# Optimization experiments

Hardware: AMD Instinct MI355X
Metric: run time of the kernel (lower is better)

## Reference

```python
import jax, jax.numpy as jnp
import numpy as np

B, T, D = 16, 1024, 768
H = 12
HD = D // H
MLP = 3072


def _layernorm(x, g, b, eps=1e-5):
    mu = jnp.mean(x, axis=-1, keepdims=True)
    var = jnp.var(x, axis=-1, keepdims=True)
    return (x - mu) * jax.lax.rsqrt(var + eps) * g + b


def setup_inputs() -> dict:
    key = jax.random.key(0)
    ks = jax.random.split(key, 12)
    s_d = 1.0 / np.sqrt(D)
    s_m = 1.0 / np.sqrt(MLP)
    return {
        "x": jax.random.normal(ks[0], (B, T, D), dtype=jnp.float32),
        "Wq": jax.random.uniform(ks[1], (D, D), jnp.float32, -s_d, s_d),
        "bq": jnp.zeros((D,), jnp.float32),
        "Wk": jax.random.uniform(ks[2], (D, D), jnp.float32, -s_d, s_d),
        "bk": jnp.zeros((D,), jnp.float32),
        "Wv": jax.random.uniform(ks[3], (D, D), jnp.float32, -s_d, s_d),
        "bv": jnp.zeros((D,), jnp.float32),
        "Wo": jax.random.uniform(ks[4], (D, D), jnp.float32, -s_d, s_d),
        "bo": jnp.zeros((D,), jnp.float32),
        "ln1_g": jnp.ones((D,), jnp.float32),
        "ln1_b": jnp.zeros((D,), jnp.float32),
        "ln2_g": jnp.ones((D,), jnp.float32),
        "ln2_b": jnp.zeros((D,), jnp.float32),
        "W1": jax.random.uniform(ks[5], (D, MLP), jnp.float32, -s_d, s_d),
        "b1": jnp.zeros((MLP,), jnp.float32),
        "W2": jax.random.uniform(ks[6], (MLP, D), jnp.float32, -s_m, s_m),
        "b2": jnp.zeros((D,), jnp.float32),
    }


def reference(x, Wq, bq, Wk, bk, Wv, bv, Wo, bo, ln1_g, ln1_b, ln2_g, ln2_b, W1, b1, W2, b2):
    h = _layernorm(x, ln1_g, ln1_b)
    # QKV projections -> [B, H, T, HD]
    q = (h @ Wq + bq).reshape(B, T, H, HD).transpose(0, 2, 1, 3)
    k = (h @ Wk + bk).reshape(B, T, H, HD).transpose(0, 2, 1, 3)
    v = (h @ Wv + bv).reshape(B, T, H, HD).transpose(0, 2, 1, 3)
    # NOTE: original divides by sqrt(input_dim), not sqrt(head_dim)
    scores = jnp.einsum('bhtf,bhjf->bhtj', q, k) / jnp.sqrt(jnp.float32(D))
    score = jax.nn.softmax(scores, axis=-1)
    attn = jnp.einsum('bhij,bhjf->bihf', score, v)  # [B, T, H, HD]
    attn_out = attn.reshape(B, T, D) @ Wo + bo
    out = attn_out + x
    h2 = _layernorm(out, ln2_g, ln2_b)
    # MLP: Linear -> GELU -> Linear -> GELU (GELU after 2nd linear is in the source)
    m = jax.nn.gelu(h2 @ W1 + b1, approximate=False)
    m = jax.nn.gelu(m @ W2 + b2, approximate=False)
    return m + out
```

## Files before the change

kernel.cpp:

```cpp
#include <hip/hip_runtime.h>
#include <hip/hip_bf16.h>
#include <math.h>

#define D_MODEL 768
#define T_SEQ   1024
#define B_BATCH 16
#define MLP_DIM 3072
#define M_ROWS  (B_BATCH * T_SEQ)

typedef __attribute__((ext_vector_type(8))) __bf16          bf16x8;
typedef __attribute__((ext_vector_type(4))) __bf16          bf16x4;
typedef __attribute__((ext_vector_type(4))) float           f32x4;

__device__ __forceinline__ float bf2f(unsigned short u) {
  union { unsigned int u; float f; } w; w.u = ((unsigned int)u) << 16; return w.f;
}
__device__ __forceinline__ unsigned short f2bf(float f) {
  union { float f; unsigned int u; } w; w.f = f;
  unsigned int r = (w.u + 0x7fffu + ((w.u >> 16) & 1u)) >> 16;
  return (unsigned short)r;
}
__device__ __forceinline__ float gelu_f(float x) {
  return 0.5f * x * (1.0f + erff(x * 0.70710678118654752f));
}
__device__ __forceinline__ void gload16(const void* g, void* l) {
  __builtin_amdgcn_global_load_lds(
      (const __attribute__((address_space(1))) unsigned int*)g,
      (__attribute__((address_space(3))) unsigned int*)l, 16, 0, 0);
}

__global__ void wtr_k(const float* __restrict__ src,
                      unsigned short* __restrict__ dst, int R, int C) {
  __shared__ float t[32][33];
  const int c0 = blockIdx.x * 32, r0 = blockIdx.y * 32;
  const int tx = threadIdx.x, ty = threadIdx.y;
  #pragma unroll
  for (int j = 0; j < 32; j += 8)
    t[ty + j][tx] = src[(size_t)(r0 + ty + j) * C + (c0 + tx)];
  __syncthreads();
  #pragma unroll
  for (int j = 0; j < 32; j += 8)
    dst[(size_t)(c0 + ty + j) * R + (r0 + tx)] = f2bf(t[tx][ty + j]);
}

__global__ void bcat_k(const float* __restrict__ a, const float* __restrict__ b,
                       const float* __restrict__ c, float* __restrict__ o) {
  const int i = blockIdx.x * 256 + threadIdx.x;
  if (i < 768) { o[i] = a[i]; o[i + 768] = b[i]; o[i + 1536] = c[i]; }
}

template<int SRC_F32>
__global__ __launch_bounds__(256) void ln_k(const void* __restrict__ src,
    const float* __restrict__ g, const float* __restrict__ b,
    unsigned short* __restrict__ out) {
  const int row = blockIdx.x, tid = threadIdx.x;
  const size_t base = (size_t)row * D_MODEL;
  float v[3];
  #pragma unroll
  for (int i = 0; i < 3; ++i) {
    const int c = tid + (i << 8);
    v[i] = SRC_F32 ? ((const float*)src)[base + c]
                   : bf2f(((const unsigned short*)src)[base + c]);
  }
  float s  = v[0] + v[1] + v[2];
  float sq = v[0]*v[0] + v[1]*v[1] + v[2]*v[2];
  #pragma unroll
  for (int m = 32; m; m >>= 1) { s += __shfl_xor(s, m); sq += __shfl_xor(sq, m); }
  __shared__ float ps[4], pq[4];
  if ((tid & 63) == 0) { ps[tid >> 6] = s; pq[tid >> 6] = sq; }
  __syncthreads();
  s  = ps[0] + ps[1] + ps[2] + ps[3];
  sq = pq[0] + pq[1] + pq[2] + pq[3];
  const float mu  = s * (1.0f / 768.0f);
  const float var = sq * (1.0f / 768.0f) - mu * mu;
  const float inv = rsqrtf(var + 1e-5f);
  #pragma unroll
  for (int i = 0; i < 3; ++i) {
    const int c = tid + (i << 8);
    out[base + c] = f2bf((v[i] - mu) * inv * g[c] + b[c]);
  }
}

template<int EP>
__global__ __launch_bounds__(256) void gemm_k(
    const unsigned short* __restrict__ Au, const unsigned short* __restrict__ Btu,
    const float* __restrict__ bias, void* __restrict__ outv,
    const void* __restrict__ residv, void* __restrict__ aux,
    int M, int N, int K, int cb, int cgrp) {
  __shared__ __align__(16) __bf16 SMEM[2 * 2 * 128 * 32];
  auto As = (__bf16 (*)[128][32])(SMEM);
  auto Bs = (__bf16 (*)[128][32])(SMEM + 2 * 128 * 32);
  const __bf16* A  = (const __bf16*)Au;
  const __bf16* Bt = (const __bf16*)Btu;
  const int tid = threadIdx.x;
  const int lane = tid & 63, wid = tid >> 6;
  const int wr = wid >> 1, wc = wid & 1;
  const int gx = gridDim.x, gy = gridDim.y;
  const int bid = blockIdx.y * gx + blockIdx.x;
  const int xcd = bid & 7, idx = bid >> 3;
  const int rpx = gx >> 3;
  const int gsz = rpx * cgrp;
  const int grp = idx / gsz, rem = idx - grp * gsz;
  const int r = rem / cgrp, c = rem - r * cgrp + grp * cgrp;
  const int brow  = (xcd * rpx + r) * 128;
  const int bcolL = c * 128;
  const int bcol  = cb + bcolL;
  const int lr = lane & 15, lg = lane >> 4;
  f32x4 acc[4][4];
  #pragma unroll
  for (int m = 0; m < 4; ++m)
    #pragma unroll
    for (int n = 0; n < 4; ++n) acc[m][n] = (f32x4){0.f, 0.f, 0.f, 0.f};

  const int srow = (wid << 5) + (lane >> 2);
  const int scol = (lane & 3) << 3;
  const __bf16* gA = A  + (size_t)(brow  + srow) * K + scol;
  const __bf16* gB = Bt + (size_t)(bcolL + srow) * K + scol;

#define STAGE_(buf_, k0_) do {                                        \
    gload16(gA + (k0_),                   &As[buf_][(wid << 5)][0]);  \
    gload16(gA + (k0_) + 16 * (size_t)K,  &As[buf_][(wid << 5) + 16][0]); \
    gload16(gB + (k0_),                   &Bs[buf_][(wid << 5)][0]);  \
    gload16(gB + (k0_) + 16 * (size_t)K,  &Bs[buf_][(wid << 5) + 16][0]); \
  } while (0)

  STAGE_(0, 0);
  int cur = 0;
  for (int k0 = 0; k0 < K; k0 += 32, cur ^= 1) {
    if (k0 + 32 < K) {
      STAGE_(cur ^ 1, k0 + 32);
      asm volatile("s_waitcnt vmcnt(4)" ::: "memory");
    } else {
      asm volatile("s_waitcnt vmcnt(0)" ::: "memory");
    }
    __builtin_amdgcn_s_barrier();
    __builtin_amdgcn_sched_barrier(0);
    bf16x8 af[4], bfr[4];
    #pragma unroll
    for (int m = 0; m < 4; ++m) af[m]  = *(const bf16x8*)(&As[cur][wr*64 + m*16 + lr][lg*8]);
    #pragma unroll
    for (int n = 0; n < 4; ++n) bfr[n] = *(const bf16x8*)(&Bs[cur][wc*64 + n*16 + lr][lg*8]);
    #pragma unroll
    for (int m = 0; m < 4; ++m)
      #pragma unroll
      for (int n = 0; n < 4; ++n)
        acc[m][n] = __builtin_amdgcn_mfma_f32_16x16x32_bf16(af[m], bfr[n], acc[m][n], 0, 0, 0);
    asm volatile("s_waitcnt lgkmcnt(0)" ::: "memory");
    __builtin_amdgcn_sched_barrier(0);
    __builtin_amdgcn_s_barrier();
    __builtin_amdgcn_sched_barrier(0);
  }
#undef STAGE_

  const int seg = (EP == 5) ? (bcol / 768) : 0;
  unsigned short* qkvp = nullptr;
  if (EP == 5)
    qkvp = (seg == 0) ? (unsigned short*)outv
         : (seg == 1) ? (unsigned short*)residv : (unsigned short*)aux;

  if (EP == 5 && seg == 2) {
    #pragma unroll
    for (int n = 0; n < 4; ++n) {
      const int col = bcol + wc*64 + n*16 + lr;
      const float bv = bias[col];
      const int colLv = col - 1536;
      #pragma unroll
      for (int m = 0; m < 4; ++m) {
        const int row0 = brow + wr*64 + m*16 + lg*4;
        #pragma unroll
        for (int r2 = 0; r2 < 4; ++r2) {
          const int gr = row0 + r2;
          qkvp[(((size_t)(gr >> 10) * D_MODEL + colLv) << 10) + (gr & 1023)] =
              f2bf(acc[m][n][r2] + bv);
        }
      }
    }
  } else {
    float* Ep = (float*)SMEM + wid * 1280;
    #pragma unroll
    for (int p = 0; p < 4; ++p) {
      #pragma unroll
      for (int n = 0; n < 4; ++n) {
        const int col = bcol + wc*64 + n*16 + lr;
        const float bv = bias[col];
        f32x4 st;
        #pragma unroll
        for (int r2 = 0; r2 < 4; ++r2) {
          float v = acc[p][n][r2] + bv;
          if (EP == 1 || EP == 3) v = gelu_f(v);
          st[r2] = v;
        }
        *(f32x4*)(Ep + (n*16 + lr) * 20 + lg*4) = st;
      }
      #pragma unroll
      for (int i2 = 0; i2 < 2; ++i2) {
        const int rowL = i2*8 + (lane >> 3);
        const int colL = (lane & 7) * 8;
        const int grow = brow + wr*64 + p*16 + rowL;
        const int gcol = bcol + wc*64 + colL;
        float v[8];
        #pragma unroll
        for (int j = 0; j < 8; ++j) v[j] = Ep[(colL + j) * 20 + rowL];
        const size_t o = (size_t)grow * N + gcol;
        if (EP == 3) {
          const bf16x8 rv = *(const bf16x8*)((const __bf16*)residv + o);
          float* op = (float*)outv + o;
          float4 o0, o1;
          o0.x = v[0] + (float)rv[0]; o0.y = v[1] + (float)rv[1];
          o0.z = v[2] + (float)rv[2]; o0.w = v[3] + (float)rv[3];
          o1.x = v[4] + (float)rv[4]; o1.y = v[5] + (float)rv[5];
          o1.z = v[6] + (float)rv[6]; o1.w = v[7] + (float)rv[7];
          *(float4*)op = o0; *(float4*)(op + 4) = o1;
        } else if (EP == 2) {
          const float* rp = (const float*)residv + o;
          const float4 r0 = *(const float4*)rp, r1 = *(const float4*)(rp + 4);
          bf16x8 ov;
          ov[0] = (__bf16)(v[0] + r0.x); ov[1] = (__bf16)(v[1] + r0.y);
          ov[2] = (__bf16)(v[2] + r0.z); ov[3] = (__bf16)(v[3] + r0.w);
          ov[4] = (__bf16)(v[4] + r1.x); ov[5] = (__bf16)(v[5] + r1.y);
          ov[6] = (__bf16)(v[6] + r1.z); ov[7] = (__bf16)(v[7] + r1.w);
          *(bf16x8*)((__bf16*)outv + o) = ov;
        } else if (EP == 5) {
          bf16x8 ov;
          #pragma unroll
          for (int j = 0; j < 8; ++j) ov[j] = (__bf16)v[j];
          *(bf16x8*)((__bf16*)qkvp + (size_t)grow * 768 + (gcol - seg * 768)) = ov;
        } else {
          bf16x8 ov;
          #pragma unroll
          for (int j = 0; j < 8; ++j) ov[j] = (__bf16)v[j];
          *(bf16x8*)((__bf16*)outv + o) = ov;
        }
      }
    }
  }
}

__global__ __launch_bounds__(512) void attn_k(
    const unsigned short* qu, const unsigned short* __restrict__ ku,
    const unsigned short* __restrict__ vtu, unsigned short* attn) {
  __shared__ __align__(16) __bf16 Kl[64][72];
  __shared__ __align__(16) __bf16 Vl[64][72];
  __shared__ __align__(16) __bf16 Pl[8][16][72];
  const __bf16* qg  = (const __bf16*)qu;
  const __bf16* kg  = (const __bf16*)ku;
  const __bf16* vtg = (const __bf16*)vtu;
  const int bid = blockIdx.x;
  const int xcd = bid & 7, idx = bid >> 3;
  const int bh = xcd * 24 + (idx >> 2);
  const int b = bh / 12, h = bh % 12;
  const int q0 = (idx & 3) * 256;
  const int tid = threadIdx.x, lane = tid & 63, w = tid >> 6;
  const int lr = lane & 15, lg = lane >> 4;
  const float scale = 0.03608439182435161f;

  bf16x8 qa[2][2];
  #pragma unroll
  for (int g = 0; g < 2; ++g) {
    const int qrow = b * T_SEQ + q0 + w * 32 + g * 16 + lr;
    const __bf16* qp = qg + (size_t)qrow * D_MODEL + h * 64 + lg * 8;
    qa[g][0] = *(const bf16x8*)(qp);
    qa[g][1] = *(const bf16x8*)(qp + 32);
  }

  const __bf16* kb = kg  + (size_t)b * T_SEQ * D_MODEL + h * 64;
  const __bf16* vb = vtg + ((size_t)b * D_MODEL + h * 64) * T_SEQ;

  f32x4 o[2][4];
  float m_run[2] = {-1e30f, -1e30f}, l_run[2] = {0.f, 0.f};
  #pragma unroll
  for (int g = 0; g < 2; ++g)
    #pragma unroll
    for (int m = 0; m < 4; ++m) o[g][m] = (f32x4){0.f, 0.f, 0.f, 0.f};

  for (int kv0 = 0; kv0 < T_SEQ; kv0 += 64) {
    __syncthreads();
    {
      const int r = tid >> 3, c = (tid & 7) << 3;
      *(bf16x8*)(&Kl[r][c]) = *(const bf16x8*)(kb + (size_t)(kv0 + r) * D_MODEL + c);
      *(bf16x8*)(&Vl[r][c]) = *(const bf16x8*)(vb + (size_t)r * T_SEQ + kv0 + c);
    }
    __syncthreads();

    #pragma unroll
    for (int g = 0; g < 2; ++g) {
      f32x4 s[4];
      __builtin_amdgcn_s_setprio(1);
      #pragma unroll
      for (int m = 0; m < 4; ++m) {
        s[m] = (f32x4){0.f, 0.f, 0.f, 0.f};
        const bf16x8 kf0 = *(const bf16x8*)(&Kl[m*16 + lr][lg*8]);
        const bf16x8 kf1 = *(const bf16x8*)(&Kl[m*16 + lr][32 + lg*8]);
        s[m] = __builtin_amdgcn_mfma_f32_16x16x32_bf16(kf0, qa[g][0], s[m], 0, 0, 0);
        s[m] = __builtin_amdgcn_mfma_f32_16x16x32_bf16(kf1, qa[g][1], s[m], 0, 0, 0);
      }
      __builtin_amdgcn_s_setprio(0);
      float sv[4][4], tm = -1e30f;
      #pragma unroll
      for (int m = 0; m < 4; ++m)
        #pragma unroll
        for (int r = 0; r < 4; ++r) {
          sv[m][r] = s[m][r] * scale;
          tm = fmaxf(tm, sv[m][r]);
        }
      tm = fmaxf(tm, __shfl_xor(tm, 16));
      tm = fmaxf(tm, __shfl_xor(tm, 32));
      const float mn = fmaxf(m_run[g], tm);
      const float sc = __expf(m_run[g] - mn);
      float ts = 0.f;
      bf16x4 pk[4];
      #pragma unroll
      for (int m = 0; m < 4; ++m)
        #pragma unroll
        for (int r = 0; r < 4; ++r) {
          const float pp = __expf(sv[m][r] - mn);
          ts += pp;
          pk[m][r] = (__bf16)pp;
        }
      ts += __shfl_xor(ts, 16);
      ts += __shfl_xor(ts, 32);
      l_run[g] = l_run[g] * sc + ts;
      m_run[g] = mn;
      #pragma unroll
      for (int m = 0; m < 4; ++m)
        #pragma unroll
        for (int r = 0; r < 4; ++r) o[g][m][r] *= sc;
      #pragma unroll
      for (int m = 0; m < 4; ++m)
        *(bf16x4*)(&Pl[w][lr][16*m + 4*lg]) = pk[m];
      const bf16x8 pf0 = *(const bf16x8*)(&Pl[w][lr][lg*8]);
      const bf16x8 pf1 = *(const bf16x8*)(&Pl[w][lr][32 + lg*8]);
      __builtin_amdgcn_s_setprio(1);
      #pragma unroll
      for (int m = 0; m < 4; ++m) {
        const bf16x8 vf0 = *(const bf16x8*)(&Vl[m*16 + lr][lg*8]);
        const bf16x8 vf1 = *(const bf16x8*)(&Vl[m*16 + lr][32 + lg*8]);
        o[g][m] = __builtin_amdgcn_mfma_f32_16x16x32_bf16(vf0, pf0, o[g][m], 0, 0, 0);
        o[g][m] = __builtin_amdgcn_mfma_f32_16x16x32_bf16(vf1, pf1, o[g][m], 0, 0, 0);
      }
      __builtin_amdgcn_s_setprio(0);
    }
  }

  #pragma unroll
  for (int g = 0; g < 2; ++g) {
    const float inv = 1.0f / l_run[g];
    const int qrow = b * T_SEQ + q0 + w * 32 + g * 16 + lr;
    unsigned short* op = attn + (size_t)qrow * D_MODEL + h * 64;
    #pragma unroll
    for (int m = 0; m < 4; ++m) {
      bf16x4 ov;
      #pragma unroll
      for (int r = 0; r < 4; ++r) ov[r] = (__bf16)(o[g][m][r] * inv);
      *(bf16x4*)(op + 16*m + 4*lg) = ov;
    }
  }
}

extern "C" void kernel_launch(void* const* d_in, const int* in_sizes, int n_in,
                              void* d_out, int out_size, void* d_ws, size_t ws_size,
                              hipStream_t stream) {
  const float* x   = (const float*)d_in[0];
  const float* Wq  = (const float*)d_in[1];
  const float* bq  = (const float*)d_in[2];
  const float* Wk  = (const float*)d_in[3];
  const float* bk  = (const float*)d_in[4];
  const float* Wv  = (const float*)d_in[5];
  const float* bv  = (const float*)d_in[6];
  const float* Wo  = (const float*)d_in[7];
  const float* bo  = (const float*)d_in[8];
  const float* g1  = (const float*)d_in[9];
  const float* bt1 = (const float*)d_in[10];
  const float* g2  = (const float*)d_in[11];
  const float* bt2 = (const float*)d_in[12];
  const float* W1  = (const float*)d_in[13];
  const float* bb1 = (const float*)d_in[14];
  const float* W2  = (const float*)d_in[15];
  const float* bb2 = (const float*)d_in[16];

  const size_t SZ = (size_t)M_ROWS * D_MODEL * 2;
  char* wp = (char*)d_ws;
  unsigned short* wqkvT = (unsigned short*)wp; wp += (size_t)2304 * 768 * 2;
  unsigned short* woT   = (unsigned short*)wp; wp += (size_t)768 * 768 * 2;
  unsigned short* w1T   = (unsigned short*)wp; wp += (size_t)768 * 3072 * 2;
  unsigned short* w2T   = (unsigned short*)wp; wp += (size_t)768 * 3072 * 2;
  float*          bqkv  = (float*)wp;          wp += ((size_t)2304 * 4 + 255) & ~(size_t)255;
  unsigned short* kbuf  = (unsigned short*)wp; wp += SZ;
  unsigned short* vtb   = (unsigned short*)wp;
  unsigned short* res2  = kbuf;
  unsigned short* hid   = vtb;
  const size_t avail = ws_size - (size_t)(wp - (char*)d_ws);
  const int nch = (avail >= (size_t)M_ROWS * MLP_DIM * 2) ? 1
                : (avail >= (size_t)(M_ROWS / 2) * MLP_DIM * 2) ? 2 : 4;

  unsigned short* qd = (unsigned short*)d_out;
  unsigned short* h1 = qd + (size_t)M_ROWS * D_MODEL;
  unsigned short* h2 = h1;

  const dim3 tb(32, 8, 1);
  wtr_k<<<dim3(24, 24), tb, 0, stream>>>(Wq, wqkvT, 768, 768);
  wtr_k<<<dim3(24, 24), tb, 0, stream>>>(Wk, wqkvT + (size_t)768 * 768, 768, 768);
  wtr_k<<<dim3(24, 24), tb, 0, stream>>>(Wv, wqkvT + (size_t)1536 * 768, 768, 768);
  wtr_k<<<dim3(24, 24), tb, 0, stream>>>(Wo, woT, 768, 768);
  wtr_k<<<dim3(96, 24), tb, 0, stream>>>(W1, w1T, 768, 3072);
  wtr_k<<<dim3(24, 96), tb, 0, stream>>>(W2, w2T, 3072, 768);
  bcat_k<<<3, 256, 0, stream>>>(bq, bk, bv, bqkv);

  ln_k<1><<<M_ROWS, 256, 0, stream>>>(x, g1, bt1, h1);

  gemm_k<5><<<dim3(128, 18), 256, 0, stream>>>(h1, wqkvT, bqkv, qd, kbuf, vtb,
                                               M_ROWS, 2304, 768, 0, 9);

  attn_k<<<dim3(768), 512, 0, stream>>>(qd, kbuf, vtb, qd);

  gemm_k<2><<<dim3(128, 6), 256, 0, stream>>>(qd, woT, bo, res2, x, nullptr,
                                              M_ROWS, 768, 768, 0, 6);

  ln_k<0><<<M_ROWS, 256, 0, stream>>>(res2, g2, bt2, h2);

  const int CH = M_ROWS / nch;
  for (int c = 0; c < nch; ++c) {
    const size_t ro = (size_t)c * CH;
    gemm_k<1><<<dim3(CH / 128, 24), 256, 0, stream>>>(h2 + ro * 768, w1T, bb1,
        hid, nullptr, nullptr, CH, 3072, 768, 0, 12);
    gemm_k<3><<<dim3(CH / 128, 6), 256, 0, stream>>>(hid, w2T, bb2,
        (float*)d_out + ro * 768, res2 + ro * 768, nullptr, CH, 768, 3072, 0, 6);
  }
}
```

Baseline: 522.7 us.

## Enlarge GEMM tiles to 256x256 with 8 waves, K-step 64, swizzled LDS

The GEMM kernel now uses 256x256 output tiles computed by 512 threads (2x4 waves, each 128x64), a K-step of 64 per stage, and an XOR-swizzled LDS layout to avoid bank conflicts. It also raises wave priority around the MFMA block. All four GEMM launches are resized to match. The goal is more data reuse per byte loaded and fewer loop iterations. The cost is much higher register pressure (128 accumulator floats per lane), larger LDS use per block, and fewer blocks, which risks poor wave balance on the smaller GEMMs.

Result: faster. 508.3 us (-2.8%).

```diff
diff --git a/kernel.cpp b/kernel.cpp
--- a/kernel.cpp
+++ b/kernel.cpp
@@ -82,69 +82,95 @@
 }
 
 template<int EP>
-__global__ __launch_bounds__(256) void gemm_k(
+__global__ __launch_bounds__(512) void gemm_k(
     const unsigned short* __restrict__ Au, const unsigned short* __restrict__ Btu,
     const float* __restrict__ bias, void* __restrict__ outv,
     const void* __restrict__ residv, void* __restrict__ aux,
-    int M, int N, int K, int cb, int cgrp) {
-  __shared__ __align__(16) __bf16 SMEM[2 * 2 * 128 * 32];
-  auto As = (__bf16 (*)[128][32])(SMEM);
-  auto Bs = (__bf16 (*)[128][32])(SMEM + 2 * 128 * 32);
+    int M, int N, int K, int cgrp) {
+  __shared__ __align__(16) __bf16 SMEM[2 * 32768];
   const __bf16* A  = (const __bf16*)Au;
   const __bf16* Bt = (const __bf16*)Btu;
   const int tid = threadIdx.x;
-  const int lane = tid & 63, wid = tid >> 6;
-  const int wr = wid >> 1, wc = wid & 1;
+  const int lane = tid & 63, w = tid >> 6;
+  const int wr = w >> 2, wc = w & 3;
+  const int lr = lane & 15, lg = lane >> 4;
   const int gx = gridDim.x, gy = gridDim.y;
   const int bid = blockIdx.y * gx + blockIdx.x;
   const int xcd = bid & 7, idx = bid >> 3;
   const int rpx = gx >> 3;
   const int gsz = rpx * cgrp;
   const int grp = idx / gsz, rem = idx - grp * gsz;
-  const int r = rem / cgrp, c = rem - r * cgrp + grp * cgrp;
-  const int brow  = (xcd * rpx + r) * 128;
-  const int bcolL = c * 128;
-  const int bcol  = cb + bcolL;
-  const int lr = lane & 15, lg = lane >> 4;
-  f32x4 acc[4][4];
-  #pragma unroll
-  for (int m = 0; m < 4; ++m)
+  const int rb = rem / cgrp, cc2 = rem - rb * cgrp + grp * cgrp;
+  const int brow = (xcd * rpx + rb) * 256;
+  const int bcol = cc2 * 256;
+
+  f32x4 acc[8][4];
+  #pragma unroll
+  for (int m = 0; m < 8; ++m)
     #pragma unroll
     for (int n = 0; n < 4; ++n) acc[m][n] = (f32x4){0.f, 0.f, 0.f, 0.f};
 
-  const int srow = (wid << 5) + (lane >> 2);
-  const int scol = (lane & 3) << 3;
-  const __bf16* gA = A  + (size_t)(brow  + srow) * K + scol;
-  const __bf16* gB = Bt + (size_t)(bcolL + srow) * K + scol;
-
-#define STAGE_(buf_, k0_) do {                                        \
-    gload16(gA + (k0_),                   &As[buf_][(wid << 5)][0]);  \
-    gload16(gA + (k0_) + 16 * (size_t)K,  &As[buf_][(wid << 5) + 16][0]); \
-    gload16(gB + (k0_),                   &Bs[buf_][(wid << 5)][0]);  \
-    gload16(gB + (k0_) + 16 * (size_t)K,  &Bs[buf_][(wid << 5) + 16][0]); \
+  const int rrs = lane >> 2;
+  const int ccs = (lane & 3) << 3;
+  const int csw = ccs ^ ((rrs >> 3) << 4);
+  const __bf16* sA[4]; const __bf16* sB[4]; int dA[4], dB[4];
+  #pragma unroll
+  for (int g = 0; g < 4; ++g) {
+    const int s = g * 8 + w;
+    const int rsrc = (s >> 1) * 16 + rrs;
+    const int csrc = (s & 1) * 32 + csw;
+    sA[g] = A  + (size_t)(brow + rsrc) * K + csrc;
+    sB[g] = Bt + (size_t)(bcol + rsrc) * K + csrc;
+    dA[g] = s * 512;
+    dB[g] = 16384 + s * 512;
+  }
+
+#define STAGE_(buf_, k0_) do {                                     \
+    _Pragma("unroll")                                              \
+    for (int g = 0; g < 4; ++g) {                                  \
+      gload16(sA[g] + (k0_), &SMEM[(buf_) * 32768 + dA[g]]);       \
+      gload16(sB[g] + (k0_), &SMEM[(buf_) * 32768 + dB[g]]);       \
+    }                                                              \
   } while (0)
+
+  const int rbase = lr * 32 + ((lg << 3) ^ (((lr >> 3) & 1) << 4));
 
   STAGE_(0, 0);
   int cur = 0;
-  for (int k0 = 0; k0 < K; k0 += 32, cur ^= 1) {
-    if (k0 + 32 < K) {
-      STAGE_(cur ^ 1, k0 + 32);
-      asm volatile("s_waitcnt vmcnt(4)" ::: "memory");
+  for (int k0 = 0; k0 < K; k0 += 64, cur ^= 1) {
+    if (k0 + 64 < K) {
+      STAGE_(cur ^ 1, k0 + 64);
+      asm volatile("s_waitcnt vmcnt(8)" ::: "memory");
     } else {
       asm volatile("s_waitcnt vmcnt(0)" ::: "memory");
     }
     __builtin_amdgcn_s_barrier();
     __builtin_amdgcn_sched_barrier(0);
-    bf16x8 af[4], bfr[4];
-    #pragma unroll
-    for (int m = 0; m < 4; ++m) af[m]  = *(const bf16x8*)(&As[cur][wr*64 + m*16 + lr][lg*8]);
-    #pragma unroll
-    for (int n = 0; n < 4; ++n) bfr[n] = *(const bf16x8*)(&Bs[cur][wc*64 + n*16 + lr][lg*8]);
-    #pragma unroll
-    for (int m = 0; m < 4; ++m)
-      #pragma unroll
-      for (int n = 0; n < 4; ++n)
-        acc[m][n] = __builtin_amdgcn_mfma_f32_16x16x32_bf16(af[m], bfr[n], acc[m][n], 0, 0, 0);
+    const int bb = cur * 32768;
+    bf16x8 bfr[4][2];
+    #pragma unroll
+    for (int n = 0; n < 4; ++n)
+      #pragma unroll
+      for (int kk = 0; kk < 2; ++kk)
+        bfr[n][kk] = *(const bf16x8*)(&SMEM[bb + 16384 + ((wc*4 + n)*2 + kk)*512 + rbase]);
+    __builtin_amdgcn_s_setprio(1);
+    #pragma unroll
+    for (int mq = 0; mq < 2; ++mq) {
+      bf16x8 af[4][2];
+      #pragma unroll
+      for (int ml = 0; ml < 4; ++ml)
+        #pragma unroll
+        for (int kk = 0; kk < 2; ++kk)
+          af[ml][kk] = *(const bf16x8*)(&SMEM[bb + ((wr*8 + mq*4 + ml)*2 + kk)*512 + rbase]);
+      #pragma unroll
+      for (int ml = 0; ml < 4; ++ml)
+        #pragma unroll
+        for (int n = 0; n < 4; ++n) {
+          acc[mq*4+ml][n] = __builtin_amdgcn_mfma_f32_16x16x32_bf16(af[ml][0], bfr[n][0], acc[mq*4+ml][n], 0, 0, 0);
+          acc[mq*4+ml][n] = __builtin_amdgcn_mfma_f32_16x16x32_bf16(af[ml][1], bfr[n][1], acc[mq*4+ml][n], 0, 0, 0);
+        }
+    }
+    __builtin_amdgcn_s_setprio(0);
     asm volatile("s_waitcnt lgkmcnt(0)" ::: "memory");
     __builtin_amdgcn_sched_barrier(0);
     __builtin_amdgcn_s_barrier();
@@ -165,8 +191,8 @@
       const float bv = bias[col];
       const int colLv = col - 1536;
       #pragma unroll
-      for (int m = 0; m < 4; ++m) {
-        const int row0 = brow + wr*64 + m*16 + lg*4;
+      for (int m = 0; m < 8; ++m) {
+        const int row0 = brow + wr*128 + m*16 + lg*4;
         #pragma unroll
         for (int r2 = 0; r2 < 4; ++r2) {
           const int gr = row0 + r2;
@@ -176,9 +202,9 @@
       }
     }
   } else {
-    float* Ep = (float*)SMEM + wid * 1280;
-    #pragma unroll
-    for (int p = 0; p < 4; ++p) {
+    float* Ep = (float*)SMEM + w * 1280;
+    #pragma unroll
+    for (int m = 0; m < 8; ++m) {
       #pragma unroll
       for (int n = 0; n < 4; ++n) {
         const int col = bcol + wc*64 + n*16 + lr;
@@ -186,7 +212,7 @@
         f32x4 st;
         #pragma unroll
         for (int r2 = 0; r2 < 4; ++r2) {
-          float v = acc[p][n][r2] + bv;
+          float v = acc[m][n][r2] + bv;
           if (EP == 1 || EP == 3) v = gelu_f(v);
           st[r2] = v;
         }
@@ -196,7 +222,7 @@
       for (int i2 = 0; i2 < 2; ++i2) {
         const int rowL = i2*8 + (lane >> 3);
         const int colL = (lane & 7) * 8;
-        const int grow = brow + wr*64 + p*16 + rowL;
+        const int grow = brow + wr*128 + m*16 + rowL;
         const int gcol = bcol + wc*64 + colL;
         float v[8];
         #pragma unroll
@@ -408,22 +434,22 @@
 
   ln_k<1><<<M_ROWS, 256, 0, stream>>>(x, g1, bt1, h1);
 
-  gemm_k<5><<<dim3(128, 18), 256, 0, stream>>>(h1, wqkvT, bqkv, qd, kbuf, vtb,
-                                               M_ROWS, 2304, 768, 0, 9);
+  gemm_k<5><<<dim3(64, 9), 512, 0, stream>>>(h1, wqkvT, bqkv, qd, kbuf, vtb,
+                                             M_ROWS, 2304, 768, 9);
 
   attn_k<<<dim3(768), 512, 0, stream>>>(qd, kbuf, vtb, qd);
 
-  gemm_k<2><<<dim3(128, 6), 256, 0, stream>>>(qd, woT, bo, res2, x, nullptr,
-                                              M_ROWS, 768, 768, 0, 6);
+  gemm_k<2><<<dim3(64, 3), 512, 0, stream>>>(qd, woT, bo, res2, x, nullptr,
+                                             M_ROWS, 768, 768, 3);
 
   ln_k<0><<<M_ROWS, 256, 0, stream>>>(res2, g2, bt2, h2);
 
   const int CH = M_ROWS / nch;
   for (int c = 0; c < nch; ++c) {
     const size_t ro = (size_t)c * CH;
-    gemm_k<1><<<dim3(CH / 128, 24), 256, 0, stream>>>(h2 + ro * 768, w1T, bb1,
-        hid, nullptr, nullptr, CH, 3072, 768, 0, 12);
-    gemm_k<3><<<dim3(CH / 128, 6), 256, 0, stream>>>(hid, w2T, bb2,
-        (float*)d_out + ro * 768, res2 + ro * 768, nullptr, CH, 768, 3072, 0, 6);
-  }
-}
+    gemm_k<1><<<dim3(CH / 256, 12), 512, 0, stream>>>(h2 + ro * 768, w1T, bb1,
+        hid, nullptr, nullptr, CH, 3072, 768, 6);
+    gemm_k<3><<<dim3(CH / 256, 3), 512, 0, stream>>>(hid, w2T, bb2,
+        (float*)d_out + ro * 768, res2 + ro * 768, nullptr, CH, 768, 3072, 3);
+  }
+}
```
